# Kernel optimization log

Hardware: AMD Instinct MI355X
Metric: run time of the kernel (lower is better)

## Reference

```python
import jax, jax.numpy as jnp
import numpy as np

DIM = 256
NUM_HEADS = 4
HEAD_DIM = DIM // NUM_HEADS
SCALE = HEAD_DIM ** -0.5


def setup_inputs() -> dict:
    key = jax.random.key(0)
    k1, k2, k3, k4 = jax.random.split(key, 4)
    B, N, C = 2, 4096, DIM
    x = jax.random.normal(k1, (B, N, C), dtype=jnp.float32)
    # nn.Linear(dim, 3*dim, bias=False): weight [3C, C], y = x @ W.T
    w_qkv = jax.random.normal(k2, (3 * C, C), dtype=jnp.float32) * (C ** -0.5)
    # nn.Linear(dim, dim) with bias
    w_proj = jax.random.normal(k3, (C, C), dtype=jnp.float32) * (C ** -0.5)
    b_proj = jax.random.normal(k4, (C,), dtype=jnp.float32) * 0.02
    return {"x": x, "w_qkv": w_qkv, "w_proj": w_proj, "b_proj": b_proj}


def reference(x, w_qkv, w_proj, b_proj):
    B, N, C = x.shape
    H, D = NUM_HEADS, HEAD_DIM
    qkv = x @ w_qkv.T                                  # [B, N, 3C]
    qkv = qkv.reshape(B, N, 3, H, D).transpose(2, 0, 3, 1, 4)  # [3, B, H, N, D]
    q, k, v = qkv[0], qkv[1], qkv[2]
    attn = jnp.einsum("bhnd,bhmd->bhnm", q, k) * SCALE  # [B, H, N, N]
    attn = jax.nn.softmax(attn, axis=-1)
    out = jnp.einsum("bhnm,bhmd->bhnd", attn, v)        # [B, H, N, D]
    out = out.transpose(0, 2, 1, 3).reshape(B, N, C)
    out = out @ w_proj.T + b_proj
    return out
```

## Files before the change

kernel.cpp:

```cpp
#include <hip/hip_runtime.h>
#include <hip/hip_bf16.h>
#include <stdint.h>

typedef __bf16 bf16;
typedef __bf16 bf16x8 __attribute__((ext_vector_type(8)));
typedef __bf16 bf16x4 __attribute__((ext_vector_type(4)));
typedef float  f32x4  __attribute__((ext_vector_type(4)));

#define MFMA16(a, b, c) __builtin_amdgcn_mfma_f32_16x16x32_bf16((a), (b), (c), 0, 0, 0)

#define BB   2
#define NN   4096
#define CC   256
#define HH   4
#define DD   64
#define BH   8
#define SL2E 0.1803368801111244f

__device__ __forceinline__ void gload_lds16(const void* g, void* l) {
    __builtin_amdgcn_global_load_lds(
        (const __attribute__((address_space(1))) void*)g,
        (__attribute__((address_space(3))) void*)l, 16, 0, 0);
}

__global__ __launch_bounds__(256) void cvt_all(const float* __restrict__ x,
                                               const float* __restrict__ wq,
                                               const float* __restrict__ wp,
                                               bf16* __restrict__ xb,
                                               bf16* __restrict__ wqb,
                                               bf16* __restrict__ wpb) {
    int i = blockIdx.x * 256 + threadIdx.x;
    const float* src; bf16* dst; int j;
    if (i < 524288)      { src = x;  dst = xb;  j = i; }
    else if (i < 573440) { src = wq; dst = wqb; j = i - 524288; }
    else if (i < 589824) { src = wp; dst = wpb; j = i - 573440; }
    else return;
    f32x4 v = ((const f32x4*)src)[j];
    bf16x4 o;
    o[0] = (bf16)v[0]; o[1] = (bf16)v[1]; o[2] = (bf16)v[2]; o[3] = (bf16)v[3];
    ((bf16x4*)dst)[j] = o;
}

__global__ __launch_bounds__(256) void gemm_qkv(const bf16* __restrict__ X,
                                                const bf16* __restrict__ W,
                                                bf16* __restrict__ Q,
                                                bf16* __restrict__ K,
                                                bf16* __restrict__ Vt) {
    const int wave = threadIdx.x >> 6;
    const int lane = threadIdx.x & 63;
    const int lr = lane & 15;
    const int lg = lane >> 4;
    const int row0 = blockIdx.x * 128 + wave * 32;
    const int col0 = blockIdx.y * 64;

    f32x4 acc[2][4] = {};
    for (int k0 = 0; k0 < 256; k0 += 32) {
        bf16x8 a[2], b[4];
#pragma unroll
        for (int i = 0; i < 2; i++)
            a[i] = *(const bf16x8*)&X[(size_t)(row0 + 16 * i + lr) * 256 + k0 + 8 * lg];
#pragma unroll
        for (int t = 0; t < 4; t++)
            b[t] = *(const bf16x8*)&W[(size_t)(col0 + 16 * t + lr) * 256 + k0 + 8 * lg];
#pragma unroll
        for (int i = 0; i < 2; i++)
#pragma unroll
            for (int t = 0; t < 4; t++)
                acc[i][t] = MFMA16(a[i], b[t], acc[i][t]);
    }

    const int s = col0 >> 8;
    const int h = (col0 >> 6) & 3;
    if (s == 2) {
#pragma unroll
        for (int i = 0; i < 2; i++) {
#pragma unroll
            for (int t = 0; t < 4; t++) {
                int row = row0 + 16 * i + 4 * lg;
                int d   = 16 * t + lr;
                int bh  = ((row >> 12) << 2) | h;
                int nb  = row & 4095;
                int g   = nb >> 5, m = (nb >> 2) & 7;
                int np  = (g << 5) + ((m & 3) << 3) + ((m >> 2) << 2);
                bf16x4 o4;
#pragma unroll
                for (int r = 0; r < 4; r++) o4[r] = (bf16)acc[i][t][r];
                *(bf16x4*)&Vt[((size_t)bh * DD + d) * NN + np] = o4;
            }
        }
    } else {
        bf16* dst = (s == 0) ? Q : K;
        const float sc = (s == 0) ? SL2E : 1.0f;
#pragma unroll
        for (int i = 0; i < 2; i++) {
#pragma unroll
            for (int t = 0; t < 4; t++) {
#pragma unroll
                for (int r = 0; r < 4; r++) {
                    int row = row0 + 16 * i + 4 * lg + r;
                    int d   = 16 * t + lr;
                    int bh  = ((row >> 12) << 2) | h;
                    int n   = row & 4095;
                    dst[((size_t)bh * NN + n) * DD + d] = (bf16)(acc[i][t][r] * sc);
                }
            }
        }
    }
}

__global__ __launch_bounds__(256) void flash_attn(const bf16* __restrict__ Q,
                                                  const bf16* __restrict__ K,
                                                  const bf16* __restrict__ Vt,
                                                  bf16* __restrict__ Op,
                                                  float* __restrict__ ps,
                                                  int nsplit) {
    __shared__ __align__(16) char kv_lds[2][16384];

    const int bh   = blockIdx.y;
    const int wave = threadIdx.x >> 6;
    const int lane = threadIdx.x & 63;
    const int lr   = lane & 15;
    const int lg   = lane >> 4;
    const int tid  = threadIdx.x;
    const int swz  = (lr & 7) << 4;

    const char* Khb  = (const char*)(K  + (size_t)bh * NN * DD);
    const char* Vthb = (const char*)(Vt + (size_t)bh * DD * NN);
    const bf16* Qh   = Q + (size_t)bh * NN * DD;

    const int qw = blockIdx.x * 128 + wave * 32;

    bf16x8 qf[2][2];
#pragma unroll
    for (int s = 0; s < 2; s++) {
        qf[s][0] = *(const bf16x8*)&Qh[(size_t)(qw + 16 * s + lr) * DD + 8 * lg];
        qf[s][1] = *(const bf16x8*)&Qh[(size_t)(qw + 16 * s + lr) * DD + 32 + 8 * lg];
    }

    const int L  = tid * 16;
    const int r0 = L >> 7;
    const int c0 = (L & 127) ^ ((r0 & 7) << 4);

    bf16x8 onesf;
#pragma unroll
    for (int j = 0; j < 8; j++) onesf[j] = (bf16)1.0f;

    f32x4 oa[2][4] = {};
    f32x4 psacc[2] = {};

    auto stage = [&](int t, char* buf) {
        const int kv0 = t * 64;
        gload_lds16(Khb + (size_t)(kv0 + r0) * 128 + c0,             buf + L);
        gload_lds16(Khb + (size_t)(kv0 + r0 + 32) * 128 + c0,        buf + 4096 + L);
        gload_lds16(Vthb + (size_t)r0 * 8192 + kv0 * 2 + c0,         buf + 8192 + L);
        gload_lds16(Vthb + (size_t)(r0 + 32) * 8192 + kv0 * 2 + c0,  buf + 12288 + L);
    };

    auto compute = [&](const char* buf) {
        const char* kb = buf;
        const char* vb = buf + 8192;

        f32x4 sacc[2][4];
        __builtin_amdgcn_s_setprio(1);
#pragma unroll
        for (int t = 0; t < 4; t++) {
            const char* rowk = kb + (16 * t + lr) * 128;
            bf16x8 kf0 = *(const bf16x8*)(rowk + ((16 * lg) ^ swz));
            bf16x8 kf1 = *(const bf16x8*)(rowk + ((64 + 16 * lg) ^ swz));
#pragma unroll
            for (int s = 0; s < 2; s++) {
                f32x4 z = {0.f, 0.f, 0.f, 0.f};
                z = MFMA16(kf0, qf[s][0], z);
                z = MFMA16(kf1, qf[s][1], z);
                sacc[s][t] = z;
            }
        }
        __builtin_amdgcn_s_setprio(0);

        bf16x8 vf[2][4];
#pragma unroll
        for (int dt = 0; dt < 4; dt++) {
            const char* rowv = vb + (16 * dt + lr) * 128;
            vf[0][dt] = *(const bf16x8*)(rowv + ((16 * lg) ^ swz));
            vf[1][dt] = *(const bf16x8*)(rowv + ((64 + 16 * lg) ^ swz));
        }

#pragma unroll
        for (int s = 0; s < 2; s++) {
            bf16x8 pb[2];
#pragma unroll
            for (int c = 0; c < 2; c++) {
#pragma unroll
                for (int u = 0; u < 2; u++) {
#pragma unroll
                    for (int r = 0; r < 4; r++) {
                        float ev = __builtin_exp2f(sacc[s][2 * c + u][r]);
                        pb[c][4 * u + r] = (bf16)ev;
                    }
                }
            }
            __builtin_amdgcn_s_setprio(1);
#pragma unroll
            for (int dt = 0; dt < 4; dt++) {
                oa[s][dt] = MFMA16(vf[0][dt], pb[0], oa[s][dt]);
                oa[s][dt] = MFMA16(vf[1][dt], pb[1], oa[s][dt]);
            }
            psacc[s] = MFMA16(onesf, pb[0], psacc[s]);
            psacc[s] = MFMA16(onesf, pb[1], psacc[s]);
            __builtin_amdgcn_s_setprio(0);
        }
    };

    const int nt = 64 / nsplit;
    const int t0 = blockIdx.z * nt;

    char* cur = &kv_lds[0][0];
    char* nxt = &kv_lds[1][0];

    stage(t0, cur);
    stage(t0 + 1, nxt);

    for (int t = 0; t < nt; t++) {
        if (t + 1 < nt) asm volatile("s_waitcnt vmcnt(4)" ::: "memory");
        else            asm volatile("s_waitcnt vmcnt(0)" ::: "memory");
        __builtin_amdgcn_s_barrier();
        compute(cur);
        asm volatile("" ::: "memory");
        __builtin_amdgcn_s_barrier();
        if (t + 2 < nt) stage(t0 + t + 2, cur);
        char* tmp = cur; cur = nxt; nxt = tmp;
    }

    const int b = bh >> 2, hd = bh & 3;
#pragma unroll
    for (int s = 0; s < 2; s++) {
        const int q = qw + 16 * s + lr;
        bf16* Oz = Op + (size_t)blockIdx.z * 8192 * 256
                      + ((size_t)b * NN + q) * CC + hd * 64;
#pragma unroll
        for (int dt = 0; dt < 4; dt++) {
            bf16x4 o4;
#pragma unroll
            for (int i = 0; i < 4; i++) o4[i] = (bf16)oa[s][dt][i];
            *(bf16x4*)&Oz[16 * dt + 4 * lg] = o4;
        }
        ps[((size_t)blockIdx.z * BH + bh) * NN + q] = psacc[s][0];
    }
}

__global__ __launch_bounds__(256) void gemm_proj(const bf16* __restrict__ Op,
                                                 const float* __restrict__ ps,
                                                 const bf16* __restrict__ W,
                                                 const float* __restrict__ bias,
                                                 float* __restrict__ Out,
                                                 int nsplit) {
    const int wave = threadIdx.x >> 6;
    const int lane = threadIdx.x & 63;
    const int lr = lane & 15;
    const int lg = lane >> 4;
    const int row0 = blockIdx.x * 128 + wave * 32;
    const int col0 = blockIdx.y * 64;

    float rinv[2][4];
#pragma unroll
    for (int i = 0; i < 2; i++) {
        int row = row0 + 16 * i + lr;
        int n = row & 4095, b = row >> 12;
#pragma unroll
        for (int h = 0; h < 4; h++) {
            float s0 = ps[(size_t)(b * 4 + h) * NN + n];
            if (nsplit == 2) s0 += ps[(size_t)(BH + b * 4 + h) * NN + n];
            rinv[i][h] = 1.0f / s0;
        }
    }

    f32x4 acc[2][4] = {};
    for (int k0 = 0; k0 < 256; k0 += 32) {
        const int h = k0 >> 6;
        bf16x8 a[2], b4[4];
#pragma unroll
        for (int i = 0; i < 2; i++) {
            size_t base = (size_t)(row0 + 16 * i + lr) * 256 + k0 + 8 * lg;
            bf16x8 u = *(const bf16x8*)&Op[base];
            const float rv = rinv[i][h];
            if (nsplit == 2) {
                bf16x8 w = *(const bf16x8*)&Op[base + (size_t)8192 * 256];
#pragma unroll
                for (int j = 0; j < 8; j++)
                    a[i][j] = (bf16)(((float)u[j] + (float)w[j]) * rv);
            } else {
#pragma unroll
                for (int j = 0; j < 8; j++)
                    a[i][j] = (bf16)((float)u[j] * rv);
            }
        }
#pragma unroll
        for (int t = 0; t < 4; t++)
            b4[t] = *(const bf16x8*)&W[(size_t)(col0 + 16 * t + lr) * 256 + k0 + 8 * lg];
#pragma unroll
        for (int i = 0; i < 2; i++)
#pragma unroll
            for (int t = 0; t < 4; t++)
                acc[i][t] = MFMA16(a[i], b4[t], acc[i][t]);
    }
#pragma unroll
    for (int t = 0; t < 4; t++) {
        float bv = bias[col0 + 16 * t + lr];
#pragma unroll
        for (int i = 0; i < 2; i++) {
#pragma unroll
            for (int r = 0; r < 4; r++) {
                int row = row0 + 16 * i + 4 * lg + r;
                Out[(size_t)row * 256 + col0 + 16 * t + lr] = acc[i][t][r] + bv;
            }
        }
    }
}

extern "C" void kernel_launch(void* const* d_in, const int* in_sizes, int n_in,
                              void* d_out, int out_size, void* d_ws, size_t ws_size,
                              hipStream_t stream) {
    const float* x      = (const float*)d_in[0];
    const float* w_qkv  = (const float*)d_in[1];
    const float* w_proj = (const float*)d_in[2];
    const float* b_proj = (const float*)d_in[3];
    float* out = (float*)d_out;

    char* ws = (char*)d_ws;
    size_t off = 0;
    auto alloc = [&](size_t bytes) { void* p = ws + off; off += (bytes + 255) & ~(size_t)255; return p; };

    bf16* xb  = (bf16*)alloc((size_t)8192 * 256 * 2);
    bf16* wqb = (bf16*)alloc((size_t)768 * 256 * 2);
    bf16* wpb = (bf16*)alloc((size_t)256 * 256 * 2);
    bf16* Qb  = (bf16*)alloc((size_t)BH * NN * DD * 2);
    bf16* Kb  = (bf16*)alloc((size_t)BH * NN * DD * 2);
    bf16* Vtb = (bf16*)alloc((size_t)BH * NN * DD * 2);
    bf16* Op  = (bf16*)alloc((size_t)2 * 8192 * 256 * 2);
    float* ps = (float*)alloc((size_t)2 * BH * NN * 4);
    const int nsplit = (ws_size >= off) ? 2 : 1;

    cvt_all<<<2304, 256, 0, stream>>>(x, w_qkv, w_proj, xb, wqb, wpb);
    gemm_qkv<<<dim3(64, 12), 256, 0, stream>>>(xb, wqb, Qb, Kb, Vtb);
    flash_attn<<<dim3(32, 8, nsplit), 256, 0, stream>>>(Qb, Kb, Vtb, Op, ps, nsplit);
    gemm_proj<<<dim3(64, 4), 256, 0, stream>>>(Op, ps, wpb, b_proj, out, nsplit);
}
```

Measured before the change: 97.54 us.

## Raise KV split to four, remap blocks to XCDs, template split count

The attention kernel is templated on the KV split count, and the host picks 4 splits when the workspace is large enough, falling back to 2 or 1. Block IDs are remapped so consecutive blocks sharing a (bh, split) KV slice land on the same XCD (id&7), which should improve L2 reuse of K/V. The KV loop is unrolled by 2 with a compile-time trip count, and the projection kernel sums NSPLIT partial outputs and denominators. More splits give more blocks (1024 instead of 512) on 256 CUs but add partial-result traffic and reduction work in gemm_proj.

New measurement: 103.7 us. +6.3%, slower.

```diff
diff --git a/kernel.cpp b/kernel.cpp
--- a/kernel.cpp
+++ b/kernel.cpp
@@ -108,15 +108,22 @@
     }
 }
 
+template<int NSPLIT>
 __global__ __launch_bounds__(256) void flash_attn(const bf16* __restrict__ Q,
                                                   const bf16* __restrict__ K,
                                                   const bf16* __restrict__ Vt,
                                                   bf16* __restrict__ Op,
-                                                  float* __restrict__ ps,
-                                                  int nsplit) {
+                                                  float* __restrict__ ps) {
     __shared__ __align__(16) char kv_lds[2][16384];
 
-    const int bh   = blockIdx.y;
+    const int id  = blockIdx.x + 32 * (blockIdx.y + 8 * blockIdx.z);
+    constexpr int CHUNK = 32 * NSPLIT;
+    const int nid = (id & 7) * CHUNK + (id >> 3);
+    const int qx  = nid & 31;
+    const int g   = nid >> 5;
+    const int bh  = g & 7;
+    const int zid = g >> 3;
+
     const int wave = threadIdx.x >> 6;
     const int lane = threadIdx.x & 63;
     const int lr   = lane & 15;
@@ -128,7 +135,7 @@
     const char* Vthb = (const char*)(Vt + (size_t)bh * DD * NN);
     const bf16* Qh   = Q + (size_t)bh * NN * DD;
 
-    const int qw = blockIdx.x * 128 + wave * 32;
+    const int qw = qx * 128 + wave * 32;
 
     bf16x8 qf[2][2];
 #pragma unroll
@@ -211,8 +218,8 @@
         }
     };
 
-    const int nt = 64 / nsplit;
-    const int t0 = blockIdx.z * nt;
+    constexpr int nt = 64 / NSPLIT;
+    const int t0 = zid * nt;
 
     char* cur = &kv_lds[0][0];
     char* nxt = &kv_lds[1][0];
@@ -220,6 +227,7 @@
     stage(t0, cur);
     stage(t0 + 1, nxt);
 
+#pragma unroll 2
     for (int t = 0; t < nt; t++) {
         if (t + 1 < nt) asm volatile("s_waitcnt vmcnt(4)" ::: "memory");
         else            asm volatile("s_waitcnt vmcnt(0)" ::: "memory");
@@ -235,7 +243,7 @@
 #pragma unroll
     for (int s = 0; s < 2; s++) {
         const int q = qw + 16 * s + lr;
-        bf16* Oz = Op + (size_t)blockIdx.z * 8192 * 256
+        bf16* Oz = Op + (size_t)zid * 8192 * 256
                       + ((size_t)b * NN + q) * CC + hd * 64;
 #pragma unroll
         for (int dt = 0; dt < 4; dt++) {
@@ -244,16 +252,16 @@
             for (int i = 0; i < 4; i++) o4[i] = (bf16)oa[s][dt][i];
             *(bf16x4*)&Oz[16 * dt + 4 * lg] = o4;
         }
-        ps[((size_t)blockIdx.z * BH + bh) * NN + q] = psacc[s][0];
-    }
-}
-
+        ps[((size_t)zid * BH + bh) * NN + q] = psacc[s][0];
+    }
+}
+
+template<int NSPLIT>
 __global__ __launch_bounds__(256) void gemm_proj(const bf16* __restrict__ Op,
                                                  const float* __restrict__ ps,
                                                  const bf16* __restrict__ W,
                                                  const float* __restrict__ bias,
-                                                 float* __restrict__ Out,
-                                                 int nsplit) {
+                                                 float* __restrict__ Out) {
     const int wave = threadIdx.x >> 6;
     const int lane = threadIdx.x & 63;
     const int lr = lane & 15;
@@ -268,8 +276,10 @@
         int n = row & 4095, b = row >> 12;
 #pragma unroll
         for (int h = 0; h < 4; h++) {
-            float s0 = ps[(size_t)(b * 4 + h) * NN + n];
-            if (nsplit == 2) s0 += ps[(size_t)(BH + b * 4 + h) * NN + n];
+            float s0 = 0.0f;
+#pragma unroll
+            for (int z = 0; z < NSPLIT; z++)
+                s0 += ps[((size_t)z * BH + b * 4 + h) * NN + n];
             rinv[i][h] = 1.0f / s0;
         }
     }
@@ -281,18 +291,16 @@
 #pragma unroll
         for (int i = 0; i < 2; i++) {
             size_t base = (size_t)(row0 + 16 * i + lr) * 256 + k0 + 8 * lg;
-            bf16x8 u = *(const bf16x8*)&Op[base];
+            float av[8] = {};
+#pragma unroll
+            for (int z = 0; z < NSPLIT; z++) {
+                bf16x8 u = *(const bf16x8*)&Op[base + (size_t)z * 8192 * 256];
+#pragma unroll
+                for (int j = 0; j < 8; j++) av[j] += (float)u[j];
+            }
             const float rv = rinv[i][h];
-            if (nsplit == 2) {
-                bf16x8 w = *(const bf16x8*)&Op[base + (size_t)8192 * 256];
-#pragma unroll
-                for (int j = 0; j < 8; j++)
-                    a[i][j] = (bf16)(((float)u[j] + (float)w[j]) * rv);
-            } else {
-#pragma unroll
-                for (int j = 0; j < 8; j++)
-                    a[i][j] = (bf16)((float)u[j] * rv);
-            }
+#pragma unroll
+            for (int j = 0; j < 8; j++) a[i][j] = (bf16)(av[j] * rv);
         }
 #pragma unroll
         for (int t = 0; t < 4; t++)
@@ -336,12 +344,26 @@
     bf16* Qb  = (bf16*)alloc((size_t)BH * NN * DD * 2);
     bf16* Kb  = (bf16*)alloc((size_t)BH * NN * DD * 2);
     bf16* Vtb = (bf16*)alloc((size_t)BH * NN * DD * 2);
-    bf16* Op  = (bf16*)alloc((size_t)2 * 8192 * 256 * 2);
-    float* ps = (float*)alloc((size_t)2 * BH * NN * 4);
-    const int nsplit = (ws_size >= off) ? 2 : 1;
+
+    const size_t opBytes = (size_t)8192 * 256 * 2;
+    const size_t psBytes = (size_t)BH * NN * 4;
+    const size_t perSplit = ((opBytes + 255) & ~(size_t)255) + ((psBytes + 255) & ~(size_t)255);
+    const size_t rem = (ws_size > off) ? (ws_size - off) : 0;
+    const int nsplit = (rem >= 4 * perSplit) ? 4 : ((rem >= 2 * perSplit) ? 2 : 1);
+
+    bf16*  Op = (bf16*)alloc(opBytes * nsplit);
+    float* ps = (float*)alloc(psBytes * nsplit);
 
     cvt_all<<<2304, 256, 0, stream>>>(x, w_qkv, w_proj, xb, wqb, wpb);
     gemm_qkv<<<dim3(64, 12), 256, 0, stream>>>(xb, wqb, Qb, Kb, Vtb);
-    flash_attn<<<dim3(32, 8, nsplit), 256, 0, stream>>>(Qb, Kb, Vtb, Op, ps, nsplit);
-    gemm_proj<<<dim3(64, 4), 256, 0, stream>>>(Op, ps, wpb, b_proj, out, nsplit);
-}
+    if (nsplit == 4) {
+        flash_attn<4><<<dim3(32, 8, 4), 256, 0, stream>>>(Qb, Kb, Vtb, Op, ps);
+        gemm_proj<4><<<dim3(64, 4), 256, 0, stream>>>(Op, ps, wpb, b_proj, out);
+    } else if (nsplit == 2) {
+        flash_attn<2><<<dim3(32, 8, 2), 256, 0, stream>>>(Qb, Kb, Vtb, Op, ps);
+        gemm_proj<2><<<dim3(64, 4), 256, 0, stream>>>(Op, ps, wpb, b_proj, out);
+    } else {
+        flash_attn<1><<<dim3(32, 8, 1), 256, 0, stream>>>(Qb, Kb, Vtb, Op, ps);
+        gemm_proj<1><<<dim3(64, 4), 256, 0, stream>>>(Op, ps, wpb, b_proj, out);
+    }
+}
```

## Drop split-KV attention and normalize output inside the flash kernel

Applied to the files above, without the earlier changes.

Removes the two-way KV split in the attention kernel, so each block now walks all 64 KV tiles. The softmax normalization moves into the attention epilogue, and the projection GEMM reads a single normalized bf16 output directly. This removes the partial-sum workspace, the extra partial-output reads and the per-row reciprocal work in the projection kernel. In exchange the attention grid halves to 256 blocks, which lowers the number of waves per CU available to hide latency.

After: 120.9 us. 1.24x slower.

```diff
diff --git a/kernel.cpp b/kernel.cpp
--- a/kernel.cpp
+++ b/kernel.cpp
@@ -111,9 +111,7 @@
 __global__ __launch_bounds__(256) void flash_attn(const bf16* __restrict__ Q,
                                                   const bf16* __restrict__ K,
                                                   const bf16* __restrict__ Vt,
-                                                  bf16* __restrict__ Op,
-                                                  float* __restrict__ ps,
-                                                  int nsplit) {
+                                                  bf16* __restrict__ O) {
     __shared__ __align__(16) char kv_lds[2][16384];
 
     const int bh   = blockIdx.y;
@@ -211,14 +209,13 @@
         }
     };
 
-    const int nt = 64 / nsplit;
-    const int t0 = blockIdx.z * nt;
+    const int nt = 64;
 
     char* cur = &kv_lds[0][0];
     char* nxt = &kv_lds[1][0];
 
-    stage(t0, cur);
-    stage(t0 + 1, nxt);
+    stage(0, cur);
+    stage(1, nxt);
 
     for (int t = 0; t < nt; t++) {
         if (t + 1 < nt) asm volatile("s_waitcnt vmcnt(4)" ::: "memory");
@@ -227,7 +224,7 @@
         compute(cur);
         asm volatile("" ::: "memory");
         __builtin_amdgcn_s_barrier();
-        if (t + 2 < nt) stage(t0 + t + 2, cur);
+        if (t + 2 < nt) stage(t + 2, cur);
         char* tmp = cur; cur = nxt; nxt = tmp;
     }
 
@@ -235,25 +232,22 @@
 #pragma unroll
     for (int s = 0; s < 2; s++) {
         const int q = qw + 16 * s + lr;
-        bf16* Oz = Op + (size_t)blockIdx.z * 8192 * 256
-                      + ((size_t)b * NN + q) * CC + hd * 64;
+        const float rinv = 1.0f / psacc[s][0];
+        bf16* Oz = O + ((size_t)b * NN + q) * CC + hd * 64;
 #pragma unroll
         for (int dt = 0; dt < 4; dt++) {
             bf16x4 o4;
 #pragma unroll
-            for (int i = 0; i < 4; i++) o4[i] = (bf16)oa[s][dt][i];
+            for (int i = 0; i < 4; i++) o4[i] = (bf16)(oa[s][dt][i] * rinv);
             *(bf16x4*)&Oz[16 * dt + 4 * lg] = o4;
         }
-        ps[((size_t)blockIdx.z * BH + bh) * NN + q] = psacc[s][0];
-    }
-}
-
-__global__ __launch_bounds__(256) void gemm_proj(const bf16* __restrict__ Op,
-                                                 const float* __restrict__ ps,
+    }
+}
+
+__global__ __launch_bounds__(256) void gemm_proj(const bf16* __restrict__ O,
                                                  const bf16* __restrict__ W,
                                                  const float* __restrict__ bias,
-                                                 float* __restrict__ Out,
-                                                 int nsplit) {
+                                                 float* __restrict__ Out) {
     const int wave = threadIdx.x >> 6;
     const int lane = threadIdx.x & 63;
     const int lr = lane & 15;
@@ -261,39 +255,12 @@
     const int row0 = blockIdx.x * 128 + wave * 32;
     const int col0 = blockIdx.y * 64;
 
-    float rinv[2][4];
-#pragma unroll
-    for (int i = 0; i < 2; i++) {
-        int row = row0 + 16 * i + lr;
-        int n = row & 4095, b = row >> 12;
-#pragma unroll
-        for (int h = 0; h < 4; h++) {
-            float s0 = ps[(size_t)(b * 4 + h) * NN + n];
-            if (nsplit == 2) s0 += ps[(size_t)(BH + b * 4 + h) * NN + n];
-            rinv[i][h] = 1.0f / s0;
-        }
-    }
-
     f32x4 acc[2][4] = {};
     for (int k0 = 0; k0 < 256; k0 += 32) {
-        const int h = k0 >> 6;
         bf16x8 a[2], b4[4];
 #pragma unroll
-        for (int i = 0; i < 2; i++) {
-            size_t base = (size_t)(row0 + 16 * i + lr) * 256 + k0 + 8 * lg;
-            bf16x8 u = *(const bf16x8*)&Op[base];
-            const float rv = rinv[i][h];
-            if (nsplit == 2) {
-                bf16x8 w = *(const bf16x8*)&Op[base + (size_t)8192 * 256];
-#pragma unroll
-                for (int j = 0; j < 8; j++)
-                    a[i][j] = (bf16)(((float)u[j] + (float)w[j]) * rv);
-            } else {
-#pragma unroll
-                for (int j = 0; j < 8; j++)
-                    a[i][j] = (bf16)((float)u[j] * rv);
-            }
-        }
+        for (int i = 0; i < 2; i++)
+            a[i] = *(const bf16x8*)&O[(size_t)(row0 + 16 * i + lr) * 256 + k0 + 8 * lg];
 #pragma unroll
         for (int t = 0; t < 4; t++)
             b4[t] = *(const bf16x8*)&W[(size_t)(col0 + 16 * t + lr) * 256 + k0 + 8 * lg];
@@ -336,12 +303,10 @@
     bf16* Qb  = (bf16*)alloc((size_t)BH * NN * DD * 2);
     bf16* Kb  = (bf16*)alloc((size_t)BH * NN * DD * 2);
     bf16* Vtb = (bf16*)alloc((size_t)BH * NN * DD * 2);
-    bf16* Op  = (bf16*)alloc((size_t)2 * 8192 * 256 * 2);
-    float* ps = (float*)alloc((size_t)2 * BH * NN * 4);
-    const int nsplit = (ws_size >= off) ? 2 : 1;
+    bf16* Ob  = (bf16*)alloc((size_t)8192 * 256 * 2);
 
     cvt_all<<<2304, 256, 0, stream>>>(x, w_qkv, w_proj, xb, wqb, wpb);
     gemm_qkv<<<dim3(64, 12), 256, 0, stream>>>(xb, wqb, Qb, Kb, Vtb);
-    flash_attn<<<dim3(32, 8, nsplit), 256, 0, stream>>>(Qb, Kb, Vtb, Op, ps, nsplit);
-    gemm_proj<<<dim3(64, 4), 256, 0, stream>>>(Op, ps, wpb, b_proj, out, nsplit);
-}
+    flash_attn<<<dim3(32, 8), 256, 0, stream>>>(Qb, Kb, Vtb, Ob);
+    gemm_proj<<<dim3(64, 4), 256, 0, stream>>>(Ob, wpb, b_proj, out);
+}
```
